# Optimization experiments

Hardware: AMD Instinct MI355X
Metric: run time of the kernel (lower is better)

The kernel has to match this reference:

```python
import jax, jax.numpy as jnp
import numpy as np

N_HEAD = 12


def _build_mask(L: int, K: int) -> np.ndarray:
    """Block mask: memory rows see [memory|state]; state row sees all;
    token rows see [memory|state] plus causal among tokens."""
    m = np.zeros((L, L), dtype=bool)
    m[:K, :K + 1] = True          # memory attends to memory + state
    m[K, :] = True                # state attends to everything
    if L > K + 1:
        T = L - K - 1
        m[K + 1:, :K + 1] = True  # tokens attend to memory + state
        m[K + 1:, K + 1:] = np.tril(np.ones((T, T), dtype=bool))  # causal
    return m


def setup_inputs() -> dict:
    key = jax.random.key(0)
    k1, k2, k3 = jax.random.split(key, 3)
    B, K, T, C = 4, 128, 2048, 768
    L = K + 1 + T  # 2177
    x = jax.random.normal(k1, (B, L, C), dtype=jnp.float32)
    W_attn = jax.random.normal(k2, (C, 3 * C), dtype=jnp.float32) * 0.02
    W_proj = jax.random.normal(k3, (C, C), dtype=jnp.float32) * 0.02
    return {"x": x, "W_attn": W_attn, "W_proj": W_proj, "mem_size": K}


def reference(x, W_attn, W_proj, mem_size):
    B, L, C = x.shape
    H = N_HEAD
    d = C // H
    K = int(mem_size)

    # QKV projection (bias=False)
    qkv = x @ W_attn                                  # (B, L, 3C)
    q, k, v = jnp.split(qkv, 3, axis=-1)
    q = q.reshape(B, L, H, d).transpose(0, 2, 1, 3)   # (B, H, L, d)
    k = k.reshape(B, L, H, d).transpose(0, 2, 1, 3)
    v = v.reshape(B, L, H, d).transpose(0, 2, 1, 3)

    mask = jnp.asarray(_build_mask(L, K))             # (L, L) bool, static
    scale = 1.0 / jnp.sqrt(jnp.asarray(d, dtype=x.dtype))
    att = jnp.einsum('bhqd,bhkd->bhqk', q, k) * scale
    att = jnp.where(mask, att, -jnp.inf)
    att = jax.nn.softmax(att, axis=-1)
    y = jnp.einsum('bhqk,bhkd->bhqd', att, v)         # (B, H, L, d)
    y = y.transpose(0, 2, 1, 3).reshape(B, L, C)
    return y @ W_proj
```

## Files before the change

### kernel.cpp

```cpp
#include <hip/hip_runtime.h>
#include <hip/hip_bf16.h>

constexpr int BATCH = 4;
constexpr int MEMK  = 128;
constexpr int CDIM  = 768;
constexpr int NH    = 12;
constexpr int HD    = 64;
constexpr int LDIM  = 2177;
constexpr int MROWS = BATCH * LDIM;
constexpr int LPAD  = 2240;

typedef __attribute__((ext_vector_type(4))) float f32x4;
typedef __attribute__((ext_vector_type(8))) short short8;
typedef __attribute__((ext_vector_type(4))) short s16x4;

__device__ __forceinline__ short f2bf(float f) {
    unsigned u = __builtin_bit_cast(unsigned, f);
    u = (u + 0x7FFFu + ((u >> 16) & 1u)) >> 16;
    return (short)u;
}
__device__ __forceinline__ float bf2f(short s) {
    unsigned u = ((unsigned)(unsigned short)s) << 16;
    return __builtin_bit_cast(float, u);
}
__device__ __forceinline__ void split2(float v, short& h, short& l) {
    h = f2bf(v);
    l = f2bf(v - bf2f(h));
}
__device__ __forceinline__ void gload16(const void* g, void* l) {
    __builtin_amdgcn_global_load_lds(
        (const __attribute__((address_space(1))) void*)g,
        (__attribute__((address_space(3))) void*)l, 16, 0, 0);
}

__global__ __launch_bounds__(256)
void convsplit_kernel(const float* __restrict__ src, short* __restrict__ h,
                      short* __restrict__ l, int n4)
{
    for (int i = blockIdx.x * blockDim.x + threadIdx.x; i < n4;
         i += gridDim.x * blockDim.x) {
        float4 v = ((const float4*)src)[i];
        short hs[4], ls[4];
        split2(v.x, hs[0], ls[0]); split2(v.y, hs[1], ls[1]);
        split2(v.z, hs[2], ls[2]); split2(v.w, hs[3], ls[3]);
        ((short4*)h)[i] = make_short4(hs[0], hs[1], hs[2], hs[3]);
        ((short4*)l)[i] = make_short4(ls[0], ls[1], ls[2], ls[3]);
    }
}

__global__ __launch_bounds__(256)
void transconv_kernel(const float* __restrict__ W, short* __restrict__ th,
                      short* __restrict__ tl, int K, int N)
{
    __shared__ float tile[32][33];
    const int k0 = blockIdx.y * 32, n0 = blockIdx.x * 32;
    const int tx = threadIdx.x & 31, ty = threadIdx.x >> 5;
#pragma unroll
    for (int j = 0; j < 4; ++j)
        tile[ty + j * 8][tx] = W[(size_t)(k0 + ty + j * 8) * N + n0 + tx];
    __syncthreads();
#pragma unroll
    for (int j = 0; j < 4; ++j) {
        float v = tile[tx][ty + j * 8];
        short hi, lo; split2(v, hi, lo);
        size_t o = (size_t)(n0 + ty + j * 8) * K + k0 + tx;
        th[o] = hi; tl[o] = lo;
    }
}

template<int EPI>
__global__ __launch_bounds__(256)
void gemm_mfma_kernel(const short* __restrict__ Ah, const short* __restrict__ Al,
                      const short* __restrict__ Bh, const short* __restrict__ Bl,
                      short* __restrict__ Qh, short* __restrict__ Ql,
                      short* __restrict__ Kh, short* __restrict__ Kl,
                      short* __restrict__ Vth, short* __restrict__ Vtl,
                      float* __restrict__ Of)
{
    constexpr int KD = 768;
    __shared__ short lds[4][128 * 32];
    const int tid  = threadIdx.x;
    const int lane = tid & 63;
    const int w    = tid >> 6;
    const int wr = w >> 1, wc = w & 1;
    const int lr = lane & 15, lg = lane >> 4;
    const int row0 = blockIdx.y * 128, col0 = blockIdx.x * 128;

    f32x4 acc[4][4];
#pragma unroll
    for (int m = 0; m < 4; ++m)
#pragma unroll
        for (int n = 0; n < 4; ++n) acc[m][n] = (f32x4){0.f, 0.f, 0.f, 0.f};

    for (int kt = 0; kt < KD / 32; ++kt) {
        const int k0 = kt * 32;
        __syncthreads();
#pragma unroll
        for (int q = 0; q < 2; ++q) {
            const int c = q * 256 + tid;
            const int r = c >> 2, s = c & 3;
            const int ar = min(row0 + r, MROWS - 1);
            const int br = col0 + r;
            const size_t aoff = (size_t)ar * KD + k0 + s * 8;
            const size_t boff = (size_t)br * KD + k0 + s * 8;
            gload16(Ah + aoff, &lds[0][c * 8]);
            gload16(Al + aoff, &lds[1][c * 8]);
            gload16(Bh + boff, &lds[2][c * 8]);
            gload16(Bl + boff, &lds[3][c * 8]);
        }
        __syncthreads();

        short8 afh[4], afl[4], bfh[4], bfl[4];
#pragma unroll
        for (int m = 0; m < 4; ++m) {
            int r = wr * 64 + m * 16 + lr;
            afh[m] = *(const short8*)&lds[0][r * 32 + lg * 8];
            afl[m] = *(const short8*)&lds[1][r * 32 + lg * 8];
        }
#pragma unroll
        for (int n = 0; n < 4; ++n) {
            int r = wc * 64 + n * 16 + lr;
            bfh[n] = *(const short8*)&lds[2][r * 32 + lg * 8];
            bfl[n] = *(const short8*)&lds[3][r * 32 + lg * 8];
        }
#pragma unroll
        for (int m = 0; m < 4; ++m)
#pragma unroll
            for (int n = 0; n < 4; ++n) {
                f32x4 a = acc[m][n];
                a = __builtin_amdgcn_mfma_f32_16x16x32_bf16(afh[m], bfh[n], a, 0, 0, 0);
                a = __builtin_amdgcn_mfma_f32_16x16x32_bf16(afl[m], bfh[n], a, 0, 0, 0);
                a = __builtin_amdgcn_mfma_f32_16x16x32_bf16(afh[m], bfl[n], a, 0, 0, 0);
                acc[m][n] = a;
            }
    }

#pragma unroll
    for (int n = 0; n < 4; ++n) {
        const int colb = col0 + wc * 64 + n * 16;
        if (EPI == 0) {
            const int sel = colb / CDIM;
            const int c0  = colb - sel * CDIM;
            const int h   = c0 >> 6;
            const int dd  = (c0 & 63) + lr;
            const float scl = (sel == 0) ? 0.125f : 1.0f;
#pragma unroll
            for (int m = 0; m < 4; ++m)
#pragma unroll
                for (int e = 0; e < 4; ++e) {
                    int mg = row0 + wr * 64 + m * 16 + lg * 4 + e;
                    if (mg >= MROWS) continue;
                    int b = mg / LDIM, l = mg - b * LDIM;
                    short hi, lo; split2(acc[m][n][e] * scl, hi, lo);
                    if (sel == 0) {
                        size_t o = (((size_t)(b * NH + h)) * LDIM + l) * HD + dd;
                        Qh[o] = hi; Ql[o] = lo;
                    } else if (sel == 1) {
                        size_t o = (((size_t)(b * NH + h)) * LDIM + l) * HD + dd;
                        Kh[o] = hi; Kl[o] = lo;
                    } else {
                        size_t o = (((size_t)(b * NH + h)) * HD + dd) * LPAD + l;
                        Vth[o] = hi; Vtl[o] = lo;
                    }
                }
        } else {
#pragma unroll
            for (int m = 0; m < 4; ++m)
#pragma unroll
                for (int e = 0; e < 4; ++e) {
                    int mg = row0 + wr * 64 + m * 16 + lg * 4 + e;
                    if (mg >= MROWS) continue;
                    Of[(size_t)mg * CDIM + colb + lr] = acc[m][n][e];
                }
        }
    }
}

__global__ __launch_bounds__(256)
void attn_mfma_kernel(const short* __restrict__ Qh, const short* __restrict__ Ql,
                      const short* __restrict__ Kh, const short* __restrict__ Kl,
                      const short* __restrict__ Vth, const short* __restrict__ Vtl,
                      short* __restrict__ Yh, short* __restrict__ Yl)
{
    __shared__ short Klds[2][64 * 64];
    __shared__ short Vlds[2][64 * 64];
    __shared__ short Pqs[4][2][32 * 64];
    const int tid  = threadIdx.x;
    const int lane = tid & 63;
    const int w    = tid >> 6;
    const int lr = lane & 15, lg = lane >> 4;
    const int bh = blockIdx.y;
    const int b = bh / NH, h = bh % NH;
    constexpr int NXB = (LDIM + 127) / 128;
    const int qb = (NXB - 1 - (int)blockIdx.x) * 128;
    const int qw = qb + w * 32;

    int mynt;
    if (qw >= LDIM) mynt = 0;
    else if (qw <= MEMK && MEMK <= qw + 31) mynt = (LDIM - 1) / 64 + 1;
    else if (qw + 31 < MEMK) mynt = MEMK / 64 + 1;
    else mynt = min(qw + 31, LDIM - 1) / 64 + 1;
    int bnt;
    if (qb <= MEMK && MEMK <= qb + 127) bnt = (LDIM - 1) / 64 + 1;
    else if (qb + 127 < MEMK) bnt = MEMK / 64 + 1;
    else bnt = min(qb + 127, LDIM - 1) / 64 + 1;

    int rkmax[2];
#pragma unroll
    for (int rg = 0; rg < 2; ++rg) {
        int q = qw + rg * 16 + lr;
        rkmax[rg] = (q < MEMK) ? MEMK : (q == MEMK) ? (LDIM - 1)
                  : (q < LDIM) ? q : -1;
    }

    short8 qfh[2][2], qfl[2][2];
#pragma unroll
    for (int rg = 0; rg < 2; ++rg)
#pragma unroll
        for (int dc = 0; dc < 2; ++dc) {
            int qr = min(qw + rg * 16 + lr, LDIM - 1);
            size_t off = ((size_t)bh * LDIM + qr) * HD + dc * 32 + lg * 8;
            qfh[rg][dc] = *(const short8*)(Qh + off);
            qfl[rg][dc] = *(const short8*)(Ql + off);
        }

    f32x4 O[2][4];
#pragma unroll
    for (int rg = 0; rg < 2; ++rg)
#pragma unroll
        for (int g = 0; g < 4; ++g) O[rg][g] = (f32x4){0.f, 0.f, 0.f, 0.f};
    float mrun[2] = {-INFINITY, -INFINITY};
    float lsum[2] = {0.f, 0.f};

    const short* Khb = Kh  + (size_t)bh * LDIM * HD;
    const short* Klb = Kl  + (size_t)bh * LDIM * HD;
    const short* Vhb = Vth + (size_t)bh * HD * LPAD;
    const short* Vlb = Vtl + (size_t)bh * HD * LPAD;

    for (int t = 0; t < bnt; ++t) {
        const int k0 = t * 64;
        __syncthreads();
#pragma unroll
        for (int it = 0; it < 2; ++it) {
            int c = it * 256 + tid;
            int row = c >> 3, j = c & 7;
            int sw = ((j ^ (row & 7)) << 3);
            gload16(Khb + (size_t)(k0 + row) * HD + sw, &Klds[0][c * 8]);
            gload16(Klb + (size_t)(k0 + row) * HD + sw, &Klds[1][c * 8]);
            gload16(Vhb + (size_t)row * LPAD + k0 + sw, &Vlds[0][c * 8]);
            gload16(Vlb + (size_t)row * LPAD + k0 + sw, &Vlds[1][c * 8]);
        }
        __syncthreads();

        if (t < mynt) {
            f32x4 S[2][4];
#pragma unroll
            for (int kg = 0; kg < 4; ++kg) {
                short8 kfh[2], kfl[2];
#pragma unroll
                for (int dc = 0; dc < 2; ++dc) {
                    int key = kg * 16 + lr;
                    int cj = (dc * 4 + lg) ^ (key & 7);
                    kfh[dc] = *(const short8*)&Klds[0][key * 64 + cj * 8];
                    kfl[dc] = *(const short8*)&Klds[1][key * 64 + cj * 8];
                }
#pragma unroll
                for (int rg = 0; rg < 2; ++rg) {
                    f32x4 a = (f32x4){0.f, 0.f, 0.f, 0.f};
#pragma unroll
                    for (int dc = 0; dc < 2; ++dc) {
                        a = __builtin_amdgcn_mfma_f32_16x16x32_bf16(kfh[dc], qfh[rg][dc], a, 0, 0, 0);
                        a = __builtin_amdgcn_mfma_f32_16x16x32_bf16(kfl[dc], qfh[rg][dc], a, 0, 0, 0);
                        a = __builtin_amdgcn_mfma_f32_16x16x32_bf16(kfh[dc], qfl[rg][dc], a, 0, 0, 0);
                    }
                    S[rg][kg] = a;
                }
            }
            float corr2[2];
#pragma unroll
            for (int rg = 0; rg < 2; ++rg) {
                const int rel = rkmax[rg] - k0 - lg * 4;
                float mx = -INFINITY;
#pragma unroll
                for (int kg = 0; kg < 4; ++kg)
#pragma unroll
                    for (int e = 0; e < 4; ++e) {
                        float v = S[rg][kg][e];
                        v = (kg * 16 + e <= rel) ? v : -INFINITY;
                        S[rg][kg][e] = v;
                        mx = fmaxf(mx, v);
                    }
                mx = fmaxf(mx, __shfl_xor(mx, 16));
                mx = fmaxf(mx, __shfl_xor(mx, 32));
                float nm = fmaxf(mrun[rg], mx);
                float corr = (nm == -INFINITY) ? 1.f : __expf(mrun[rg] - nm);
                mrun[rg] = nm;
                float ps = 0.f;
                const int qq = rg * 16 + lr;
#pragma unroll
                for (int kg = 0; kg < 4; ++kg) {
                    s16x4 h4, l4;
#pragma unroll
                    for (int e = 0; e < 4; ++e) {
                        float v = S[rg][kg][e];
                        float pp = (v == -INFINITY) ? 0.f : __expf(v - nm);
                        ps += pp;
                        short hh, ll; split2(pp, hh, ll);
                        h4[e] = hh; l4[e] = ll;
                    }
                    int c8 = (kg * 4 + lg) ^ (qq & 7);
                    *(s16x4*)&Pqs[w][0][qq * 64 + c8 * 4] = h4;
                    *(s16x4*)&Pqs[w][1][qq * 64 + c8 * 4] = l4;
                }
                ps += __shfl_xor(ps, 16);
                ps += __shfl_xor(ps, 32);
                lsum[rg] = lsum[rg] * corr + ps;
                corr2[rg] = corr;
            }
#pragma unroll
            for (int rg = 0; rg < 2; ++rg)
#pragma unroll
                for (int e = 0; e < 4; ++e) {
                    float cc = __shfl(corr2[rg], lg * 4 + e);
#pragma unroll
                    for (int ddg = 0; ddg < 4; ++ddg) O[rg][ddg][e] *= cc;
                }
#pragma unroll
            for (int kkc = 0; kkc < 2; ++kkc) {
                short8 ph[2], pl[2];
#pragma unroll
                for (int rg = 0; rg < 2; ++rg) {
                    const int qq = rg * 16 + lr, s = qq & 7;
                    const int c0 = kkc * 8 + lg * 2;
                    s16x4 a0 = *(const s16x4*)&Pqs[w][0][qq * 64 + ((c0) ^ s) * 4];
                    s16x4 a1 = *(const s16x4*)&Pqs[w][0][qq * 64 + ((c0 + 1) ^ s) * 4];
                    s16x4 b0 = *(const s16x4*)&Pqs[w][1][qq * 64 + ((c0) ^ s) * 4];
                    s16x4 b1 = *(const s16x4*)&Pqs[w][1][qq * 64 + ((c0 + 1) ^ s) * 4];
                    short8 p8, q8;
#pragma unroll
                    for (int e = 0; e < 4; ++e) {
                        p8[e] = a0[e]; p8[4 + e] = a1[e];
                        q8[e] = b0[e]; q8[4 + e] = b1[e];
                    }
                    ph[rg] = p8; pl[rg] = q8;
                }
#pragma unroll
                for (int ddg = 0; ddg < 4; ++ddg) {
                    int d = ddg * 16 + lr;
                    int cj = (kkc * 4 + lg) ^ (d & 7);
                    short8 vh = *(const short8*)&Vlds[0][d * 64 + cj * 8];
                    short8 vl = *(const short8*)&Vlds[1][d * 64 + cj * 8];
#pragma unroll
                    for (int rg = 0; rg < 2; ++rg) {
                        f32x4 a = O[rg][ddg];
                        a = __builtin_amdgcn_mfma_f32_16x16x32_bf16(ph[rg], vh, a, 0, 0, 0);
                        a = __builtin_amdgcn_mfma_f32_16x16x32_bf16(ph[rg], vl, a, 0, 0, 0);
                        a = __builtin_amdgcn_mfma_f32_16x16x32_bf16(pl[rg], vh, a, 0, 0, 0);
                        O[rg][ddg] = a;
                    }
                }
            }
        }
    }
#pragma unroll
    for (int rg = 0; rg < 2; ++rg) {
        float invv = (lsum[rg] > 0.f) ? 1.f / lsum[rg] : 0.f;
#pragma unroll
        for (int e = 0; e < 4; ++e) {
            float ie = __shfl(invv, lg * 4 + e);
            int q = qw + rg * 16 + lg * 4 + e;
            if (q < LDIM) {
#pragma unroll
                for (int ddg = 0; ddg < 4; ++ddg) {
                    float v = O[rg][ddg][e] * ie;
                    short hi, lo; split2(v, hi, lo);
                    size_t o = ((size_t)b * LDIM + q) * CDIM + h * HD + ddg * 16 + lr;
                    Yh[o] = hi; Yl[o] = lo;
                }
            }
        }
    }
}

extern "C" void kernel_launch(void* const* d_in, const int* in_sizes, int n_in,
                              void* d_out, int out_size, void* d_ws, size_t ws_size,
                              hipStream_t stream)
{
    const float* x      = (const float*)d_in[0];
    const float* W_attn = (const float*)d_in[1];
    const float* W_proj = (const float*)d_in[2];
    float* out = (float*)d_out;

    const size_t xN  = (size_t)MROWS * CDIM;
    const size_t waN = (size_t)CDIM * 3 * CDIM;
    const size_t wpN = (size_t)CDIM * CDIM;
    const size_t qkN = (size_t)BATCH * NH * LDIM * HD;
    const size_t vtN = (size_t)BATCH * NH * HD * LPAD;

    char* p = (char*)d_ws;
    short* Xh  = (short*)p; p += xN * 2;
    short* Xl  = (short*)p; p += xN * 2;
    short* Wth = (short*)p; p += waN * 2;
    short* Wtl = (short*)p; p += waN * 2;
    short* Pth = (short*)p; p += wpN * 2;
    short* Ptl = (short*)p; p += wpN * 2;
    short* Qh  = (short*)p; p += qkN * 2;
    short* Ql  = (short*)p; p += qkN * 2;
    short* Kh  = (short*)p; p += qkN * 2;
    short* Kl  = (short*)p; p += qkN * 2;
    short* Vth = (short*)p; p += vtN * 2;
    short* Vtl = (short*)p; p += vtN * 2;
    short* Yh = Xh;
    short* Yl = Xl;

    convsplit_kernel<<<2048, 256, 0, stream>>>(x, Xh, Xl, (int)(xN / 4));
    transconv_kernel<<<dim3(3 * CDIM / 32, CDIM / 32), 256, 0, stream>>>(
        W_attn, Wth, Wtl, CDIM, 3 * CDIM);
    transconv_kernel<<<dim3(CDIM / 32, CDIM / 32), 256, 0, stream>>>(
        W_proj, Pth, Ptl, CDIM, CDIM);

    gemm_mfma_kernel<0><<<dim3(3 * CDIM / 128, (MROWS + 127) / 128), 256, 0, stream>>>(
        Xh, Xl, Wth, Wtl, Qh, Ql, Kh, Kl, Vth, Vtl, nullptr);

    attn_mfma_kernel<<<dim3((LDIM + 127) / 128, BATCH * NH), 256, 0, stream>>>(
        Qh, Ql, Kh, Kl, Vth, Vtl, Yh, Yl);

    gemm_mfma_kernel<1><<<dim3(CDIM / 128, (MROWS + 127) / 128), 256, 0, stream>>>(
        Yh, Yl, Pth, Ptl, nullptr, nullptr, nullptr, nullptr, nullptr, nullptr, out);
}
```

Measured before the change: 531.5 us.

## Keep softmax probabilities in registers instead of round-tripping through LDS

The attention kernel no longer writes the split hi/lo probability tiles to a per-wave LDS buffer and reads them back. It feeds the MFMA accumulator layout straight from registers and reorders the keys consumed by the PV MFMA so the register layout lines up, reading V from LDS in matching 4-element halves. This drops the LDS traffic and the Pqs allocation, which frees shared memory. A launch-bounds occupancy hint of 4 is added, and K row loads are clamped to avoid reading past the sequence end. The risks are higher register pressure under the occupancy cap, and more but smaller LDS reads for V.

```diff
diff --git a/kernel.cpp b/kernel.cpp
--- a/kernel.cpp
+++ b/kernel.cpp
@@ -176,7 +176,7 @@
     }
 }
 
-__global__ __launch_bounds__(256)
+__global__ __launch_bounds__(256, 4)
 void attn_mfma_kernel(const short* __restrict__ Qh, const short* __restrict__ Ql,
                       const short* __restrict__ Kh, const short* __restrict__ Kl,
                       const short* __restrict__ Vth, const short* __restrict__ Vtl,
@@ -184,7 +184,6 @@
 {
     __shared__ short Klds[2][64 * 64];
     __shared__ short Vlds[2][64 * 64];
-    __shared__ short Pqs[4][2][32 * 64];
     const int tid  = threadIdx.x;
     const int lane = tid & 63;
     const int w    = tid >> 6;
@@ -245,8 +244,9 @@
             int c = it * 256 + tid;
             int row = c >> 3, j = c & 7;
             int sw = ((j ^ (row & 7)) << 3);
-            gload16(Khb + (size_t)(k0 + row) * HD + sw, &Klds[0][c * 8]);
-            gload16(Klb + (size_t)(k0 + row) * HD + sw, &Klds[1][c * 8]);
+            int krow = min(k0 + row, LDIM - 1);
+            gload16(Khb + (size_t)krow * HD + sw, &Klds[0][c * 8]);
+            gload16(Klb + (size_t)krow * HD + sw, &Klds[1][c * 8]);
             gload16(Vhb + (size_t)row * LPAD + k0 + sw, &Vlds[0][c * 8]);
             gload16(Vlb + (size_t)row * LPAD + k0 + sw, &Vlds[1][c * 8]);
         }
@@ -277,6 +277,7 @@
                 }
             }
             float corr2[2];
+            s16x4 pah[2][4], pal[2][4];
 #pragma unroll
             for (int rg = 0; rg < 2; ++rg) {
                 const int rel = rkmax[rg] - k0 - lg * 4;
@@ -296,22 +297,16 @@
                 float corr = (nm == -INFINITY) ? 1.f : __expf(mrun[rg] - nm);
                 mrun[rg] = nm;
                 float ps = 0.f;
-                const int qq = rg * 16 + lr;
-#pragma unroll
-                for (int kg = 0; kg < 4; ++kg) {
-                    s16x4 h4, l4;
+#pragma unroll
+                for (int kg = 0; kg < 4; ++kg)
 #pragma unroll
                     for (int e = 0; e < 4; ++e) {
                         float v = S[rg][kg][e];
                         float pp = (v == -INFINITY) ? 0.f : __expf(v - nm);
                         ps += pp;
                         short hh, ll; split2(pp, hh, ll);
-                        h4[e] = hh; l4[e] = ll;
-                    }
-                    int c8 = (kg * 4 + lg) ^ (qq & 7);
-                    *(s16x4*)&Pqs[w][0][qq * 64 + c8 * 4] = h4;
-                    *(s16x4*)&Pqs[w][1][qq * 64 + c8 * 4] = l4;
-                }
+                        pah[rg][kg][e] = hh; pal[rg][kg][e] = ll;
+                    }
                 ps += __shfl_xor(ps, 16);
                 ps += __shfl_xor(ps, 32);
                 lsum[rg] = lsum[rg] * corr + ps;
@@ -326,36 +321,40 @@
                     for (int ddg = 0; ddg < 4; ++ddg) O[rg][ddg][e] *= cc;
                 }
 #pragma unroll
-            for (int kkc = 0; kkc < 2; ++kkc) {
-                short8 ph[2], pl[2];
-#pragma unroll
-                for (int rg = 0; rg < 2; ++rg) {
-                    const int qq = rg * 16 + lr, s = qq & 7;
-                    const int c0 = kkc * 8 + lg * 2;
-                    s16x4 a0 = *(const s16x4*)&Pqs[w][0][qq * 64 + ((c0) ^ s) * 4];
-                    s16x4 a1 = *(const s16x4*)&Pqs[w][0][qq * 64 + ((c0 + 1) ^ s) * 4];
-                    s16x4 b0 = *(const s16x4*)&Pqs[w][1][qq * 64 + ((c0) ^ s) * 4];
-                    s16x4 b1 = *(const s16x4*)&Pqs[w][1][qq * 64 + ((c0 + 1) ^ s) * 4];
-                    short8 p8, q8;
+            for (int m = 0; m < 2; ++m) {
+                short8 Ph[2], Pl[2];
+#pragma unroll
+                for (int rg = 0; rg < 2; ++rg)
 #pragma unroll
                     for (int e = 0; e < 4; ++e) {
-                        p8[e] = a0[e]; p8[4 + e] = a1[e];
-                        q8[e] = b0[e]; q8[4 + e] = b1[e];
-                    }
-                    ph[rg] = p8; pl[rg] = q8;
-                }
+                        Ph[rg][e]     = pah[rg][2 * m][e];
+                        Ph[rg][4 + e] = pah[rg][2 * m + 1][e];
+                        Pl[rg][e]     = pal[rg][2 * m][e];
+                        Pl[rg][4 + e] = pal[rg][2 * m + 1][e];
+                    }
 #pragma unroll
                 for (int ddg = 0; ddg < 4; ++ddg) {
-                    int d = ddg * 16 + lr;
-                    int cj = (kkc * 4 + lg) ^ (d & 7);
-                    short8 vh = *(const short8*)&Vlds[0][d * 64 + cj * 8];
-                    short8 vl = *(const short8*)&Vlds[1][d * 64 + cj * 8];
+                    const int dd = ddg * 16 + lr;
+                    const int s7 = dd & 7;
+                    const int ch0 = (4 * m + (lg >> 1)) ^ s7;
+                    const int ch1 = (4 * m + 2 + (lg >> 1)) ^ s7;
+                    const int hw = (lg & 1) * 4;
+                    s16x4 va0 = *(const s16x4*)&Vlds[0][dd * 64 + ch0 * 8 + hw];
+                    s16x4 va1 = *(const s16x4*)&Vlds[0][dd * 64 + ch1 * 8 + hw];
+                    s16x4 vb0 = *(const s16x4*)&Vlds[1][dd * 64 + ch0 * 8 + hw];
+                    s16x4 vb1 = *(const s16x4*)&Vlds[1][dd * 64 + ch1 * 8 + hw];
+                    short8 vh, vl;
+#pragma unroll
+                    for (int e = 0; e < 4; ++e) {
+                        vh[e] = va0[e]; vh[4 + e] = va1[e];
+                        vl[e] = vb0[e]; vl[4 + e] = vb1[e];
+                    }
 #pragma unroll
                     for (int rg = 0; rg < 2; ++rg) {
                         f32x4 a = O[rg][ddg];
-                        a = __builtin_amdgcn_mfma_f32_16x16x32_bf16(ph[rg], vh, a, 0, 0, 0);
-                        a = __builtin_amdgcn_mfma_f32_16x16x32_bf16(ph[rg], vl, a, 0, 0, 0);
-                        a = __builtin_amdgcn_mfma_f32_16x16x32_bf16(pl[rg], vh, a, 0, 0, 0);
+                        a = __builtin_amdgcn_mfma_f32_16x16x32_bf16(Ph[rg], vh, a, 0, 0, 0);
+                        a = __builtin_amdgcn_mfma_f32_16x16x32_bf16(Ph[rg], vl, a, 0, 0, 0);
+                        a = __builtin_amdgcn_mfma_f32_16x16x32_bf16(Pl[rg], vh, a, 0, 0, 0);
                         O[rg][ddg] = a;
                     }
                 }
```

New measurement: 661.5 us. 1.24x slower.
